# Performance work log

Measured on AMD Instinct MI355X. Metric: run time of the kernel, lower is better.

The kernel has to match this reference:

```python
import jax, jax.numpy as jnp
import numpy as np

NUM_HEADS = 8
EPS = 1e-12  # matches torch F.normalize eps


def setup_inputs() -> dict:
    key = jax.random.key(0)
    ks = jax.random.split(key, 4)
    B, C, H, W = 32, 384, 32, 32
    x = jax.random.normal(ks[0], (B, C, H, W), dtype=jnp.float32)
    w_qkv = jax.random.normal(ks[1], (3 * C, C), dtype=jnp.float32) * (1.0 / np.sqrt(C))
    b_qkv = jnp.zeros((3 * C,), dtype=jnp.float32)
    temperature = jnp.ones((NUM_HEADS, 1, 1), dtype=jnp.float32)
    w_proj = jax.random.normal(ks[2], (C, C), dtype=jnp.float32) * (1.0 / np.sqrt(C))
    b_proj = jnp.zeros((C,), dtype=jnp.float32)
    return {"x": x, "w_qkv": w_qkv, "b_qkv": b_qkv, "temperature": temperature,
            "w_proj": w_proj, "b_proj": b_proj}


def _l2norm_tokens(t):
    # L2-normalize over the token axis N (last dim), torch F.normalize semantics
    n = jnp.sqrt(jnp.sum(t * t, axis=-1, keepdims=True))
    return t / jnp.maximum(n, EPS)


def reference(x, w_qkv, b_qkv, temperature, w_proj, b_proj):
    B, C, H, W = x.shape
    N = H * W
    nh = NUM_HEADS
    dh = C // nh
    xf = x.reshape(B, C, N)
    # 1x1 conv == channel GEMM: [B,3C,N]
    qkv = jnp.einsum('oc,bcn->bon', w_qkv, xf) + b_qkv[:, None]
    qkv = qkv.reshape(B, 3, nh, dh, N)
    q, k, v = qkv[:, 0], qkv[:, 1], qkv[:, 2]  # each [B,nh,dh,N]
    q = _l2norm_tokens(q)
    k = _l2norm_tokens(k)
    # cross-covariance: contract over N -> small [B,nh,dh,dh]
    attn = jnp.einsum('bhdn,bhen->bhde', q, k) * temperature
    attn = jax.nn.softmax(attn, axis=-1)
    out = jnp.einsum('bhde,bhen->bhdn', attn, v).reshape(B, C, N)
    out = jnp.einsum('oc,bcn->bon', w_proj, out) + b_proj[:, None]
    return x + out.reshape(B, C, H, W)
```

## Files before the change

kernel.cpp:

```cpp
#include <hip/hip_runtime.h>
#include <hip/hip_bf16.h>
#include <stdint.h>

#define BATCH  32
#define CDIM   384
#define NTOK   1024
#define NHEADS 8
#define DH     48

using f32x4  = __attribute__((ext_vector_type(4))) float;
using bf16x8 = __attribute__((ext_vector_type(8))) short;
using u16x4  = __attribute__((ext_vector_type(4))) uint16_t;
using u16x8  = __attribute__((ext_vector_type(8))) uint16_t;

__device__ __forceinline__ uint16_t f2bf(float f) {
  uint32_t x = __float_as_uint(f);
  uint32_t r = (x + 0x7fffu + ((x >> 16) & 1u)) >> 16;
  return (uint16_t)r;
}
__device__ __forceinline__ float bf2f(uint16_t u) {
  return __uint_as_float(((uint32_t)u) << 16);
}

#define GLL16(gsrc, ldst)                                                    \
  __builtin_amdgcn_global_load_lds(                                          \
      (const __attribute__((address_space(1))) void*)(gsrc),                 \
      (__attribute__((address_space(3))) void*)(ldst), 16, 0, 0)

__global__ __launch_bounds__(256) void k_transpose_x(const float* __restrict__ x,
                                                     uint16_t* __restrict__ xT,
                                                     uint16_t* __restrict__ xbf,
                                                     int use_xbf,
                                                     const float* __restrict__ wqkv,
                                                     const float* __restrict__ wproj,
                                                     uint16_t* __restrict__ wq,
                                                     uint16_t* __restrict__ wp) {
  int tid = threadIdx.x;
  if (blockIdx.y == 6) {
    int id = blockIdx.x + 16 * blockIdx.z;
    int n1 = 3 * CDIM * CDIM, n2 = CDIM * CDIM;
    for (int i = id * 256 + tid; i < n1 + n2; i += 512 * 256) {
      if (i < n1) wq[i] = f2bf(wqkv[i]);
      else        wp[i - n1] = f2bf(wproj[i - n1]);
    }
    return;
  }
  __shared__ float t[64][65];
  int n0 = blockIdx.x * 64;
  int c0 = blockIdx.y * 64;
  int b  = blockIdx.z;
  const float* xb = x + (size_t)b * CDIM * NTOK;
  uint16_t* xbb = xbf + (size_t)b * CDIM * NTOK;
#pragma unroll
  for (int p = 0; p < 4; ++p) {
    int r  = (tid >> 4) + p * 16;
    int cc = (tid & 15) * 4;
    float4 v = *(const float4*)(xb + (size_t)(c0 + r) * NTOK + n0 + cc);
    t[r][cc + 0] = v.x; t[r][cc + 1] = v.y; t[r][cc + 2] = v.z; t[r][cc + 3] = v.w;
    if (use_xbf) {
      u16x4 o; o[0] = f2bf(v.x); o[1] = f2bf(v.y); o[2] = f2bf(v.z); o[3] = f2bf(v.w);
      *(u16x4*)(xbb + (size_t)(c0 + r) * NTOK + n0 + cc) = o;
    }
  }
  __syncthreads();
  uint16_t* xTb = xT + (size_t)b * NTOK * CDIM;
#pragma unroll
  for (int p = 0; p < 2; ++p) {
    int n  = (tid >> 3) + p * 32;
    int cb = (tid & 7) * 8;
    u16x8 o;
#pragma unroll
    for (int j = 0; j < 8; ++j) o[j] = f2bf(t[cb + j][n]);
    *(u16x8*)(xTb + (size_t)(n0 + n) * CDIM + c0 + cb) = o;
  }
}

__device__ __forceinline__ void gemm_tile_128(const uint16_t* __restrict__ A,
                                              const uint16_t* __restrict__ B,
                                              uint16_t* ldsA, uint16_t* ldsB,
                                              f32x4 acc[4][4], int tid) {
  const int K = 384;
  int w = tid >> 6, lane = tid & 63;
  int wr = w >> 1, wc = w & 1;
  int lr = lane & 15, g = lane >> 4;
  for (int kt = 0; kt < K; kt += 64) {
    __syncthreads();
#pragma unroll
    for (int iss = 0; iss < 4; ++iss) {
      int ch = tid + 256 * iss;
      int r  = ch >> 3;
      int cs = (((ch & 7) ^ (r & 7)) << 3);
      GLL16(A + (size_t)r * K + kt + cs, ldsA + (size_t)ch * 8);
      GLL16(B + (size_t)r * K + kt + cs, ldsB + (size_t)ch * 8);
    }
    __syncthreads();
#pragma unroll
    for (int ks = 0; ks < 2; ++ks) {
      bf16x8 af[4], bfr[4];
#pragma unroll
      for (int mt = 0; mt < 4; ++mt) {
        int row = wr * 64 + mt * 16 + lr;
        int sl  = (((ks * 4 + g) ^ (row & 7)) << 3);
        af[mt] = *(const bf16x8*)(ldsA + (size_t)row * 64 + sl);
      }
#pragma unroll
      for (int nt = 0; nt < 4; ++nt) {
        int row = wc * 64 + nt * 16 + lr;
        int sl  = (((ks * 4 + g) ^ (row & 7)) << 3);
        bfr[nt] = *(const bf16x8*)(ldsB + (size_t)row * 64 + sl);
      }
#pragma unroll
      for (int mt = 0; mt < 4; ++mt)
#pragma unroll
        for (int nt = 0; nt < 4; ++nt)
          acc[mt][nt] = __builtin_amdgcn_mfma_f32_16x16x32_bf16(af[mt], bfr[nt], acc[mt][nt], 0, 0, 0);
    }
  }
}

__global__ __launch_bounds__(256) void k_qkv(const uint16_t* __restrict__ Wq,
                                             const uint16_t* __restrict__ xT,
                                             const float* __restrict__ bqkv,
                                             uint16_t* __restrict__ qk,
                                             uint16_t* __restrict__ vT) {
  __shared__ uint16_t ldsA[128 * 64];
  __shared__ uint16_t ldsB[128 * 64];
  int tid = threadIdx.x;
  int id  = blockIdx.x;
  int xcd = id & 7, idx = id >> 3;
  int jt  = xcd * 32 + (idx & 31);
  int bm  = idx >> 5;
  int o0 = bm * 128, j0 = jt * 128;
  f32x4 acc[4][4];
#pragma unroll
  for (int i = 0; i < 4; ++i)
#pragma unroll
    for (int j = 0; j < 4; ++j) acc[i][j] = (f32x4){0.f, 0.f, 0.f, 0.f};

  gemm_tile_128(Wq + (size_t)o0 * 384, xT + (size_t)j0 * 384, ldsA, ldsB, acc, tid);

  int w = tid >> 6, lane = tid & 63;
  int wr = w >> 1, wc = w & 1, lr = lane & 15, g = lane >> 4;
#pragma unroll
  for (int mt = 0; mt < 4; ++mt) {
    int ob = o0 + wr * 64 + mt * 16 + g * 4;
    float b0 = bqkv[ob + 0], b1 = bqkv[ob + 1], b2 = bqkv[ob + 2], b3 = bqkv[ob + 3];
#pragma unroll
    for (int nt = 0; nt < 4; ++nt) {
      int j = j0 + wc * 64 + nt * 16 + lr;
      int b = j >> 10, n = j & 1023;
      f32x4 v = acc[mt][nt];
      float v0 = v[0] + b0, v1 = v[1] + b1, v2 = v[2] + b2, v3 = v[3] + b3;
      if (ob < 768) {
        uint16_t* dst = qk + ((size_t)(b * 768 + ob) * 1024 + n);
        dst[0] = f2bf(v0); dst[1024] = f2bf(v1); dst[2048] = f2bf(v2); dst[3072] = f2bf(v3);
      } else {
        int oc = ob - 768;
        int h = oc / 48, d = oc % 48;
        u16x4 p;
        p[0] = f2bf(v0); p[1] = f2bf(v1); p[2] = f2bf(v2); p[3] = f2bf(v3);
        *(u16x4*)(vT + ((size_t)((b * 8 + h) * 1024 + n) * 48 + d)) = p;
      }
    }
  }
}

__global__ __launch_bounds__(512) void k_attn(const uint16_t* __restrict__ qk,
                                              const uint16_t* __restrict__ vT,
                                              const float* __restrict__ temperature,
                                              uint16_t* __restrict__ aT) {
  __shared__ float Sp[8][48][49];
  __shared__ float Sf[48][49];
  __shared__ uint16_t P[48][72];
  __shared__ float nrm[96];
  int tid = threadIdx.x, w = tid >> 6, lane = tid & 63;
  int bh = blockIdx.x, b = bh >> 3, h = bh & 7;
  const uint16_t* qbase = qk + (size_t)(b * 768 + h * 48) * 1024;
  const uint16_t* kbase = qbase + (size_t)384 * 1024;

  for (int r = w; r < 96; r += 8) {
    const uint16_t* row = (r < 48) ? (qbase + (size_t)r * 1024)
                                   : (kbase + (size_t)(r - 48) * 1024);
    float s = 0.f;
#pragma unroll
    for (int jj = 0; jj < 4; ++jj) {
      u16x4 u = *(const u16x4*)(row + (size_t)(jj * 64 + lane) * 4);
#pragma unroll
      for (int e = 0; e < 4; ++e) { float f = bf2f(u[e]); s += f * f; }
    }
#pragma unroll
    for (int off = 32; off > 0; off >>= 1) s += __shfl_down(s, off);
    if (lane == 0) nrm[r] = fmaxf(sqrtf(s), 1e-12f);
  }

  int lr = lane & 15, g = lane >> 4;
  int nbase = w * 128;
  f32x4 sacc[3][3];
#pragma unroll
  for (int i = 0; i < 3; ++i)
#pragma unroll
    for (int j = 0; j < 3; ++j) sacc[i][j] = (f32x4){0.f, 0.f, 0.f, 0.f};
#pragma unroll
  for (int ks = 0; ks < 4; ++ks) {
    bf16x8 aq[3], bk[3];
#pragma unroll
    for (int mt = 0; mt < 3; ++mt)
      aq[mt] = *(const bf16x8*)(qbase + (size_t)(mt * 16 + lr) * 1024 + nbase + ks * 32 + g * 8);
#pragma unroll
    for (int et = 0; et < 3; ++et)
      bk[et] = *(const bf16x8*)(kbase + (size_t)(et * 16 + lr) * 1024 + nbase + ks * 32 + g * 8);
#pragma unroll
    for (int mt = 0; mt < 3; ++mt)
#pragma unroll
      for (int et = 0; et < 3; ++et)
        sacc[mt][et] = __builtin_amdgcn_mfma_f32_16x16x32_bf16(aq[mt], bk[et], sacc[mt][et], 0, 0, 0);
  }
#pragma unroll
  for (int mt = 0; mt < 3; ++mt)
#pragma unroll
    for (int et = 0; et < 3; ++et)
#pragma unroll
      for (int r = 0; r < 4; ++r)
        Sp[w][mt * 16 + g * 4 + r][et * 16 + lr] = sacc[mt][et][r];
  __syncthreads();

  float temp = temperature[h];
  for (int idx = tid; idx < 48 * 48; idx += 512) {
    int d = idx / 48, e = idx - d * 48;
    float s = 0.f;
#pragma unroll
    for (int ww = 0; ww < 8; ++ww) s += Sp[ww][d][e];
    Sf[d][e] = s * temp / (nrm[d] * nrm[48 + e]);
  }
  __syncthreads();

  if (tid < 48) {
    int d = tid;
    float m = -1e30f;
    for (int e = 0; e < 48; ++e) m = fmaxf(m, Sf[d][e]);
    float sum = 0.f;
    for (int e = 0; e < 48; ++e) { float v = __expf(Sf[d][e] - m); sum += v; Sf[d][e] = v; }
    float inv = 1.f / sum;
    for (int e = 0; e < 48; ++e) P[d][e] = f2bf(Sf[d][e] * inv);
    for (int e = 48; e < 64; ++e) P[d][e] = 0;
  }
  __syncthreads();

  bf16x8 af[3][2];
#pragma unroll
  for (int mt = 0; mt < 3; ++mt)
#pragma unroll
    for (int ks = 0; ks < 2; ++ks)
      af[mt][ks] = *(const bf16x8*)(&P[mt * 16 + lr][ks * 32 + g * 8]);
  const uint16_t* vb = vT + (size_t)(b * 8 + h) * 1024 * 48;
  bf16x8 zf;
#pragma unroll
  for (int i = 0; i < 8; ++i) zf[i] = 0;
#pragma unroll
  for (int nt = 0; nt < 8; ++nt) {
    int n = w * 128 + nt * 16 + lr;
    bf16x8 bv[2];
    bv[0] = *(const bf16x8*)(vb + (size_t)n * 48 + g * 8);
    int eb1 = 32 + g * 8;
    bv[1] = (eb1 < 48) ? *(const bf16x8*)(vb + (size_t)n * 48 + eb1) : zf;
    f32x4 o[3];
#pragma unroll
    for (int mt = 0; mt < 3; ++mt) o[mt] = (f32x4){0.f, 0.f, 0.f, 0.f};
#pragma unroll
    for (int ks = 0; ks < 2; ++ks)
#pragma unroll
      for (int mt = 0; mt < 3; ++mt)
        o[mt] = __builtin_amdgcn_mfma_f32_16x16x32_bf16(af[mt][ks], bv[ks], o[mt], 0, 0, 0);
#pragma unroll
    for (int mt = 0; mt < 3; ++mt) {
      int c = h * 48 + mt * 16 + g * 4;
      u16x4 p;
#pragma unroll
      for (int r = 0; r < 4; ++r) p[r] = f2bf(o[mt][r]);
      *(u16x4*)(aT + ((size_t)(b * 1024 + n) * 384 + c)) = p;
    }
  }
}

__global__ __launch_bounds__(256) void k_proj(const uint16_t* __restrict__ Wp,
                                              const uint16_t* __restrict__ aT,
                                              const float* __restrict__ bproj,
                                              const uint16_t* __restrict__ xbf,
                                              const float* __restrict__ x,
                                              float* __restrict__ out,
                                              int use_xbf) {
  __shared__ uint16_t ldsA[128 * 64];
  __shared__ uint16_t ldsB[128 * 64];
  int tid = threadIdx.x;
  int id  = blockIdx.x;
  int xcd = id & 7, idx = id >> 3;
  int jt  = xcd * 32 + (idx & 31);
  int bm  = idx >> 5;
  int o0 = bm * 128, j0 = jt * 128;
  f32x4 acc[4][4];
#pragma unroll
  for (int i = 0; i < 4; ++i)
#pragma unroll
    for (int j = 0; j < 4; ++j) acc[i][j] = (f32x4){0.f, 0.f, 0.f, 0.f};

  gemm_tile_128(Wp + (size_t)o0 * 384, aT + (size_t)j0 * 384, ldsA, ldsB, acc, tid);

  int w = tid >> 6, lane = tid & 63;
  int wr = w >> 1, wc = w & 1, lr = lane & 15, g = lane >> 4;
#pragma unroll
  for (int mt = 0; mt < 4; ++mt) {
    int ob = o0 + wr * 64 + mt * 16 + g * 4;
    float b0 = bproj[ob + 0], b1 = bproj[ob + 1], b2 = bproj[ob + 2], b3 = bproj[ob + 3];
#pragma unroll
    for (int nt = 0; nt < 4; ++nt) {
      int j = j0 + wc * 64 + nt * 16 + lr;
      int b = j >> 10, n = j & 1023;
      f32x4 v = acc[mt][nt];
      size_t i0 = (size_t)(b * 384 + ob) * 1024 + n;
      float r0, r1, r2, r3;
      if (use_xbf) {
        r0 = bf2f(xbf[i0]); r1 = bf2f(xbf[i0 + 1024]);
        r2 = bf2f(xbf[i0 + 2048]); r3 = bf2f(xbf[i0 + 3072]);
      } else {
        r0 = x[i0]; r1 = x[i0 + 1024]; r2 = x[i0 + 2048]; r3 = x[i0 + 3072];
      }
      out[i0]        = v[0] + b0 + r0;
      out[i0 + 1024] = v[1] + b1 + r1;
      out[i0 + 2048] = v[2] + b2 + r2;
      out[i0 + 3072] = v[3] + b3 + r3;
    }
  }
}

extern "C" void kernel_launch(void* const* d_in, const int* in_sizes, int n_in,
                              void* d_out, int out_size, void* d_ws, size_t ws_size,
                              hipStream_t stream) {
  const float* x     = (const float*)d_in[0];
  const float* wqkv  = (const float*)d_in[1];
  const float* bqkv  = (const float*)d_in[2];
  const float* temp  = (const float*)d_in[3];
  const float* wproj = (const float*)d_in[4];
  const float* bproj = (const float*)d_in[5];
  float* out = (float*)d_out;

  char* ws = (char*)d_ws;
  size_t off = 0;
  auto alloc = [&](size_t bytes) -> char* {
    char* p = ws + off;
    off += (bytes + 255) & ~(size_t)255;
    return p;
  };
  uint16_t* xT    = (uint16_t*)alloc((size_t)BATCH * NTOK * CDIM * 2);
  uint16_t* wq_bf = (uint16_t*)alloc((size_t)3 * CDIM * CDIM * 2);
  uint16_t* wp_bf = (uint16_t*)alloc((size_t)CDIM * CDIM * 2);
  uint16_t* qkbuf = (uint16_t*)alloc((size_t)BATCH * 768 * NTOK * 2);
  uint16_t* vTbuf = (uint16_t*)alloc((size_t)BATCH * NHEADS * NTOK * DH * 2);
  size_t xbf_bytes = (size_t)BATCH * CDIM * NTOK * 2;
  int use_xbf = (off + xbf_bytes <= ws_size) ? 1 : 0;
  uint16_t* xbf = use_xbf ? (uint16_t*)alloc(xbf_bytes) : (uint16_t*)xT;
  uint16_t* aT  = xT;

  k_transpose_x<<<dim3(NTOK / 64, 7, BATCH), dim3(256), 0, stream>>>(
      x, xT, xbf, use_xbf, wqkv, wproj, wq_bf, wp_bf);
  k_qkv<<<dim3(2304), dim3(256), 0, stream>>>(wq_bf, xT, bqkv, qkbuf, vTbuf);
  k_attn<<<dim3(256), dim3(512), 0, stream>>>(qkbuf, vTbuf, temp, aT);
  k_proj<<<dim3(768), dim3(256), 0, stream>>>(wp_bf, aT, bproj, xbf, x, out, use_xbf);
}
```

Measured before the change: 125.3 us.

## Double-buffer QKV GEMM with larger 128x256 tiles and 512 threads

Rewrites the QKV projection kernel to use a 128x256 output tile per block with 8 waves, and double-buffers the LDS K-slices so global-to-LDS loads for the next step overlap the MFMA work on the current one. This halves the block count and raises reuse of the weight tile, and it leaves one barrier per K step instead of two. In exchange it uses 96KB of LDS per block, which may limit occupancy to one block per CU. The projection kernel keeps the old single-buffered tile routine.

```diff
diff --git a/kernel.cpp b/kernel.cpp
--- a/kernel.cpp
+++ b/kernel.cpp
@@ -75,72 +75,85 @@
   }
 }
 
-__device__ __forceinline__ void gemm_tile_128(const uint16_t* __restrict__ A,
-                                              const uint16_t* __restrict__ B,
-                                              uint16_t* ldsA, uint16_t* ldsB,
-                                              f32x4 acc[4][4], int tid) {
-  const int K = 384;
-  int w = tid >> 6, lane = tid & 63;
-  int wr = w >> 1, wc = w & 1;
-  int lr = lane & 15, g = lane >> 4;
-  for (int kt = 0; kt < K; kt += 64) {
-    __syncthreads();
-#pragma unroll
-    for (int iss = 0; iss < 4; ++iss) {
-      int ch = tid + 256 * iss;
-      int r  = ch >> 3;
-      int cs = (((ch & 7) ^ (r & 7)) << 3);
-      GLL16(A + (size_t)r * K + kt + cs, ldsA + (size_t)ch * 8);
-      GLL16(B + (size_t)r * K + kt + cs, ldsB + (size_t)ch * 8);
-    }
-    __syncthreads();
-#pragma unroll
-    for (int ks = 0; ks < 2; ++ks) {
-      bf16x8 af[4], bfr[4];
-#pragma unroll
-      for (int mt = 0; mt < 4; ++mt) {
-        int row = wr * 64 + mt * 16 + lr;
-        int sl  = (((ks * 4 + g) ^ (row & 7)) << 3);
-        af[mt] = *(const bf16x8*)(ldsA + (size_t)row * 64 + sl);
-      }
-#pragma unroll
-      for (int nt = 0; nt < 4; ++nt) {
-        int row = wc * 64 + nt * 16 + lr;
-        int sl  = (((ks * 4 + g) ^ (row & 7)) << 3);
-        bfr[nt] = *(const bf16x8*)(ldsB + (size_t)row * 64 + sl);
-      }
-#pragma unroll
-      for (int mt = 0; mt < 4; ++mt)
-#pragma unroll
-        for (int nt = 0; nt < 4; ++nt)
-          acc[mt][nt] = __builtin_amdgcn_mfma_f32_16x16x32_bf16(af[mt], bfr[nt], acc[mt][nt], 0, 0, 0);
-    }
-  }
-}
-
-__global__ __launch_bounds__(256) void k_qkv(const uint16_t* __restrict__ Wq,
+__device__ __forceinline__ void qkv_stage(const uint16_t* __restrict__ A,
+                                          const uint16_t* __restrict__ B,
+                                          uint16_t* buf, int kt, int tid) {
+  uint16_t* lA = buf;
+  uint16_t* lB = buf + 8192;
+#pragma unroll
+  for (int i = 0; i < 2; ++i) {
+    int ch = tid + 512 * i;
+    int r  = ch >> 3;
+    int cs = (((ch & 7) ^ (r & 7)) << 3);
+    GLL16(A + (size_t)r * 384 + kt + cs, lA + (size_t)ch * 8);
+  }
+#pragma unroll
+  for (int i = 0; i < 4; ++i) {
+    int ch = tid + 512 * i;
+    int r  = ch >> 3;
+    int cs = (((ch & 7) ^ (r & 7)) << 3);
+    GLL16(B + (size_t)r * 384 + kt + cs, lB + (size_t)ch * 8);
+  }
+}
+
+__global__ __launch_bounds__(512) void k_qkv(const uint16_t* __restrict__ Wq,
                                              const uint16_t* __restrict__ xT,
                                              const float* __restrict__ bqkv,
                                              uint16_t* __restrict__ qk,
                                              uint16_t* __restrict__ vT) {
-  __shared__ uint16_t ldsA[128 * 64];
-  __shared__ uint16_t ldsB[128 * 64];
+  __shared__ uint16_t lds[2][24576];
   int tid = threadIdx.x;
   int id  = blockIdx.x;
   int xcd = id & 7, idx = id >> 3;
-  int jt  = xcd * 32 + (idx & 31);
-  int bm  = idx >> 5;
-  int o0 = bm * 128, j0 = jt * 128;
+  int jt  = xcd * 16 + (idx & 15);
+  int bm  = idx >> 4;
+  int o0 = bm * 128, j0 = jt * 256;
+  const uint16_t* A = Wq + (size_t)o0 * 384;
+  const uint16_t* B = xT + (size_t)j0 * 384;
+
+  int w = tid >> 6, lane = tid & 63;
+  int wr = w >> 2, wc = w & 3;
+  int lr = lane & 15, g = lane >> 4;
+
   f32x4 acc[4][4];
 #pragma unroll
   for (int i = 0; i < 4; ++i)
 #pragma unroll
     for (int j = 0; j < 4; ++j) acc[i][j] = (f32x4){0.f, 0.f, 0.f, 0.f};
 
-  gemm_tile_128(Wq + (size_t)o0 * 384, xT + (size_t)j0 * 384, ldsA, ldsB, acc, tid);
-
-  int w = tid >> 6, lane = tid & 63;
-  int wr = w >> 1, wc = w & 1, lr = lane & 15, g = lane >> 4;
+  qkv_stage(A, B, lds[0], 0, tid);
+  asm volatile("s_waitcnt vmcnt(0)" ::: "memory");
+  __builtin_amdgcn_s_barrier();
+#pragma unroll
+  for (int t = 0; t < 6; ++t) {
+    if (t < 5) qkv_stage(A, B, lds[(t + 1) & 1], (t + 1) * 64, tid);
+    const uint16_t* lA = &lds[t & 1][0];
+    const uint16_t* lB = &lds[t & 1][8192];
+#pragma unroll
+    for (int ks = 0; ks < 2; ++ks) {
+      bf16x8 af[4], bfr[4];
+#pragma unroll
+      for (int mt = 0; mt < 4; ++mt) {
+        int row = wr * 64 + mt * 16 + lr;
+        int sl  = (((ks * 4 + g) ^ (row & 7)) << 3);
+        af[mt] = *(const bf16x8*)(lA + (size_t)row * 64 + sl);
+      }
+#pragma unroll
+      for (int nt = 0; nt < 4; ++nt) {
+        int row = wc * 64 + nt * 16 + lr;
+        int sl  = (((ks * 4 + g) ^ (row & 7)) << 3);
+        bfr[nt] = *(const bf16x8*)(lB + (size_t)row * 64 + sl);
+      }
+#pragma unroll
+      for (int mt = 0; mt < 4; ++mt)
+#pragma unroll
+        for (int nt = 0; nt < 4; ++nt)
+          acc[mt][nt] = __builtin_amdgcn_mfma_f32_16x16x32_bf16(af[mt], bfr[nt], acc[mt][nt], 0, 0, 0);
+    }
+    asm volatile("s_waitcnt vmcnt(0)" ::: "memory");
+    __builtin_amdgcn_s_barrier();
+  }
+
 #pragma unroll
   for (int mt = 0; mt < 4; ++mt) {
     int ob = o0 + wr * 64 + mt * 16 + g * 4;
@@ -161,6 +174,49 @@
         p[0] = f2bf(v0); p[1] = f2bf(v1); p[2] = f2bf(v2); p[3] = f2bf(v3);
         *(u16x4*)(vT + ((size_t)((b * 8 + h) * 1024 + n) * 48 + d)) = p;
       }
+    }
+  }
+}
+
+__device__ __forceinline__ void gemm_tile_128(const uint16_t* __restrict__ A,
+                                              const uint16_t* __restrict__ B,
+                                              uint16_t* ldsA, uint16_t* ldsB,
+                                              f32x4 acc[4][4], int tid) {
+  const int K = 384;
+  int w = tid >> 6, lane = tid & 63;
+  int wr = w >> 1, wc = w & 1;
+  int lr = lane & 15, g = lane >> 4;
+  for (int kt = 0; kt < K; kt += 64) {
+    __syncthreads();
+#pragma unroll
+    for (int iss = 0; iss < 4; ++iss) {
+      int ch = tid + 256 * iss;
+      int r  = ch >> 3;
+      int cs = (((ch & 7) ^ (r & 7)) << 3);
+      GLL16(A + (size_t)r * K + kt + cs, ldsA + (size_t)ch * 8);
+      GLL16(B + (size_t)r * K + kt + cs, ldsB + (size_t)ch * 8);
+    }
+    __syncthreads();
+#pragma unroll
+    for (int ks = 0; ks < 2; ++ks) {
+      bf16x8 af[4], bfr[4];
+#pragma unroll
+      for (int mt = 0; mt < 4; ++mt) {
+        int row = wr * 64 + mt * 16 + lr;
+        int sl  = (((ks * 4 + g) ^ (row & 7)) << 3);
+        af[mt] = *(const bf16x8*)(ldsA + (size_t)row * 64 + sl);
+      }
+#pragma unroll
+      for (int nt = 0; nt < 4; ++nt) {
+        int row = wc * 64 + nt * 16 + lr;
+        int sl  = (((ks * 4 + g) ^ (row & 7)) << 3);
+        bfr[nt] = *(const bf16x8*)(ldsB + (size_t)row * 64 + sl);
+      }
+#pragma unroll
+      for (int mt = 0; mt < 4; ++mt)
+#pragma unroll
+        for (int nt = 0; nt < 4; ++nt)
+          acc[mt][nt] = __builtin_amdgcn_mfma_f32_16x16x32_bf16(af[mt], bfr[nt], acc[mt][nt], 0, 0, 0);
     }
   }
 }
@@ -362,7 +418,7 @@
 
   k_transpose_x<<<dim3(NTOK / 64, 7, BATCH), dim3(256), 0, stream>>>(
       x, xT, xbf, use_xbf, wqkv, wproj, wq_bf, wp_bf);
-  k_qkv<<<dim3(2304), dim3(256), 0, stream>>>(wq_bf, xT, bqkv, qkbuf, vTbuf);
+  k_qkv<<<dim3(1152), dim3(512), 0, stream>>>(wq_bf, xT, bqkv, qkbuf, vTbuf);
   k_attn<<<dim3(256), dim3(512), 0, stream>>>(qkbuf, vTbuf, temp, aT);
   k_proj<<<dim3(768), dim3(256), 0, stream>>>(wp_bf, aT, bproj, xbf, x, out, use_xbf);
 }
```

Result: slower. 132.4 us (+5.7%).
